# Optimization experiments

Hardware: AMD Instinct MI355X
Metric: run time of the kernel (lower is better)

The kernel has to match this reference:

```python
import jax, jax.numpy as jnp
import numpy as np

N = 30000      # num_nodes
R0 = 8         # original relations
R = 2 * R0 + 1 # with inverses + self-loop relation = 17
IN = 256
OUT = 256
E = 300000     # original triples
NB = 8         # num_bases


def setup_inputs() -> dict:
    key = jax.random.key(0)
    k1, k2, k3, k4, k5, k6 = jax.random.split(key, 6)
    s = jax.random.randint(k1, (E,), 0, N)
    r = jax.random.randint(k2, (E,), 0, R0)
    o = jax.random.randint(k3, (E,), 0, N)
    triples = jnp.stack([s, r, o], axis=1)  # [E,3] int
    features = jax.random.normal(k4, (N, IN), dtype=jnp.float32)
    bases = jax.random.normal(k5, (NB, IN, OUT), dtype=jnp.float32) * 0.02
    comps = jax.random.normal(k6, (R, NB), dtype=jnp.float32) * 0.02
    bias = jnp.zeros((OUT,), dtype=jnp.float32)
    return {"triples": triples, "features": features, "bases": bases, "comps": comps, "bias": bias}


def reference(triples, features, bases, comps, bias):
    # basis decomposition: weights[r] = sum_b comps[r,b] * bases[b]
    weights = jnp.einsum('rb,bio->rio', comps, bases)  # [R, IN, OUT]

    s, r, o = triples[:, 0], triples[:, 1], triples[:, 2]
    nodes = jnp.arange(N)
    # eval mode: self_loop_keep_prob = 1 -> all N self loops kept
    src = jnp.concatenate([s, o, nodes])                                  # [E + E + N]
    rel = jnp.concatenate([r, r + R0, jnp.full((N,), 2 * R0, r.dtype)])
    dst = jnp.concatenate([o, s, nodes])

    # horizontal stacking: adj is [N, R*N]; row = src, col = rel*N + dst
    cols = rel * N + dst
    # column normalisation (row_normalisation=False branch of sum_sparse)
    col_sums = jnp.zeros((R * N,), jnp.float32).at[cols].add(1.0)
    sums = col_sums[cols]
    # reorder: swap normalizers of original and inverse edge blocks
    sums = jnp.concatenate([sums[E:2 * E], sums[:E], sums[2 * E:]])
    vals = 1.0 / sums

    # fw[r*N + n] = features[n] @ weights[r]
    fw = jnp.einsum('ni,rio->rno', features, weights).reshape(R * N, OUT)
    msgs = vals[:, None] * fw[cols]                    # [num_edges, OUT]
    out = jnp.zeros((N, OUT), jnp.float32).at[src].add(msgs)
    return out + bias
```

## Files before the change

### kernel.cpp

```cpp
#include <hip/hip_runtime.h>


namespace {
constexpr int kN     = 30000;
constexpr int kR0    = 8;
constexpr int kNRel  = 16;
constexpr int kIN    = 256;
constexpr int kOUT   = 256;
constexpr int kE     = 300000;
constexpr int kNB    = 8;
constexpr int kKT    = kNB * kIN;
constexpr int kRows  = kN * kNRel;
constexpr int kMsgs  = 2 * kE;
constexpr int kScanBlk  = 1024;
constexpr int kNScanBlk = (kRows + kScanBlk - 1) / kScanBlk;
constexpr int kBM    = 64;
constexpr int kMB    = (kN + kBM - 1) / kBM;
constexpr int kMPad  = kMB * kBM;
constexpr int kTN    = 16;
}

typedef __bf16 bf16x8 __attribute__((ext_vector_type(8)));
typedef float  f32x4  __attribute__((ext_vector_type(4)));
typedef unsigned int u32;

static __device__ __forceinline__ ushort f2bf(float x) {
  unsigned u = __float_as_uint(x);
  u += 0x7FFF + ((u >> 16) & 1);
  return (ushort)(u >> 16);
}

static __device__ __forceinline__ void gload16(const void* g, void* l) {
  __builtin_amdgcn_global_load_lds(
      (const __attribute__((address_space(1))) u32*)g,
      (__attribute__((address_space(3))) u32*)l, 16, 0, 0);
}


__global__ void k_prep(const float* __restrict__ f, ushort* __restrict__ fb,
                       const int* __restrict__ t, int* __restrict__ deg) {
  int i = blockIdx.x * 256 + threadIdx.x;
  if (i < kN * kIN / 4) {
    float4 v = reinterpret_cast<const float4*>(f)[i];
    ushort4 p;
    p.x = f2bf(v.x); p.y = f2bf(v.y); p.z = f2bf(v.z); p.w = f2bf(v.w);
    reinterpret_cast<ushort4*>(fb)[i] = p;
  }
  if (i < kE) {
    int s = t[3*i], r = t[3*i+1], o = t[3*i+2];
    atomicAdd(&deg[s * kNRel + r], 1);
    atomicAdd(&deg[o * kNRel + kR0 + r], 1);
  }
}

__global__ void k_bt(const float* __restrict__ bases, ushort* __restrict__ Bt) {
  __shared__ float tile[16][256];
  int b = blockIdx.x;
  int t = threadIdx.x;
#pragma unroll
  for (int kk = 0; kk < 16; ++kk)
    tile[kk][t] = bases[(size_t)(b * 16 + kk) * kOUT + t];
  __syncthreads();
  char* dst = (char*)Bt + (size_t)t * 4096;
  int xr = (t & 7) << 4;
#pragma unroll
  for (int q = 0; q < 4; ++q) {
    ushort4 p;
    p.x = f2bf(tile[q*4+0][t]); p.y = f2bf(tile[q*4+1][t]);
    p.z = f2bf(tile[q*4+2][t]); p.w = f2bf(tile[q*4+3][t]);
    *reinterpret_cast<ushort4*>(dst + ((b * 32 + q * 8) ^ xr)) = p;
  }
}


__global__ void k_scan1(const int* __restrict__ deg, int* __restrict__ rp,
                        int* __restrict__ blksum) {
  __shared__ int s[256];
  int tid = threadIdx.x;
  int base = blockIdx.x * kScanBlk + tid * 4;
  int v0 = 0, v1 = 0, v2 = 0, v3 = 0;
  if (base + 3 < kRows) {
    v0 = deg[base]; v1 = deg[base+1]; v2 = deg[base+2]; v3 = deg[base+3];
  } else {
    if (base     < kRows) v0 = deg[base];
    if (base + 1 < kRows) v1 = deg[base+1];
    if (base + 2 < kRows) v2 = deg[base+2];
  }
  int t0 = v0, t1 = t0 + v1, t2 = t1 + v2, t3 = t2 + v3;
  s[tid] = t3;
  __syncthreads();
  for (int off = 1; off < 256; off <<= 1) {
    int x = 0;
    if (tid >= off) x = s[tid - off];
    __syncthreads();
    s[tid] += x;
    __syncthreads();
  }
  int excl = tid ? s[tid-1] : 0;
  if (base     < kRows) rp[base]   = excl;
  if (base + 1 < kRows) rp[base+1] = excl + t0;
  if (base + 2 < kRows) rp[base+2] = excl + t1;
  if (base + 3 < kRows) rp[base+3] = excl + t2;
  if (tid == 255) blksum[blockIdx.x] = s[255];
}

__global__ void k_scan2(int* __restrict__ blksum) {
  __shared__ int s[512];
  int tid = threadIdx.x;
  s[tid] = (tid < kNScanBlk) ? blksum[tid] : 0;
  __syncthreads();
  for (int off = 1; off < 512; off <<= 1) {
    int x = 0;
    if (tid >= off) x = s[tid - off];
    __syncthreads();
    s[tid] += x;
    __syncthreads();
  }
  if (tid < kNScanBlk) blksum[tid] = tid ? s[tid-1] : 0;
}

__global__ void k_scan3(int* __restrict__ rp, const int* __restrict__ blksum) {
  int i = blockIdx.x * 256 + threadIdx.x;
  if (i < kRows)       rp[i] += blksum[i >> 10];
  else if (i == kRows) rp[i]  = kMsgs;
}

__global__ void k_scatter(const int* __restrict__ t, const int* __restrict__ rp,
                          int* __restrict__ deg, int* __restrict__ col) {
  int m = blockIdx.x * 256 + threadIdx.x;
  if (m >= kMsgs) return;
  int e = (m < kE) ? m : m - kE;
  int s = t[3*e], r = t[3*e+1], o = t[3*e+2];
  int rr, tn, sn;
  if (m < kE) { rr = r;        tn = s; sn = o; }
  else        { rr = kR0 + r;  tn = o; sn = s; }
  int idx = tn * kNRel + rr;
  int pos = rp[idx] + (atomicSub(&deg[idx], 1) - 1);
  col[pos] = (rr << 16) | sn;
}

#define FMA4(A, S, G) \
  A.x += (S) * G.x; A.y += (S) * G.y; A.z += (S) * G.z; A.w += (S) * G.w;


__global__ __launch_bounds__(256, 4)
void k_agg1(const int* __restrict__ rp, const int* __restrict__ col,
            const float* __restrict__ feat, const ushort* __restrict__ featbf,
            const float* __restrict__ comps, ushort* __restrict__ aggb) {
  __shared__ float cvb[4][17][kNB];
  int wv   = threadIdx.x >> 6;
  int lane = threadIdx.x & 63;
  int node = blockIdx.x * 4 + wv;

  if (lane < 17) {
    float val = 0.f;
    if (lane < kNRel) {
      int idx = node * kNRel + lane;
      int d = rp[idx + 1] - rp[idx];
      val = d > 0 ? 1.0f / (float)d : 0.f;
    }
#pragma unroll
    for (int b = 0; b < kNB; ++b)
      cvb[wv][lane][b] = comps[lane * kNB + b] * val;
  }
  __syncthreads();

  int e0 = rp[node * kNRel];
  int e1 = rp[node * kNRel + kNRel];

  float4 f = *reinterpret_cast<const float4*>(feat + (size_t)node * kIN + lane * 4);
  float4 acc[kNB];
#pragma unroll
  for (int b = 0; b < kNB; ++b) {
    float cs = comps[2*kR0*kNB + b];
    acc[b].x = cs * f.x; acc[b].y = cs * f.y; acc[b].z = cs * f.z; acc[b].w = cs * f.w;
  }

  const float4* cvr = reinterpret_cast<const float4*>(&cvb[wv][0][0]);
  const int pad = (16 << 16);

  int cc0[4], cc1[4];
  uint2 g0[4];
#pragma unroll
  for (int j = 0; j < 4; ++j) {
    int ee = e0 + j;
    int v  = col[ee < kMsgs ? ee : kMsgs - 1];
    cc0[j] = ee < e1 ? v : pad;
  }
#pragma unroll
  for (int j = 0; j < 4; ++j)
    g0[j] = *reinterpret_cast<const uint2*>(featbf + (size_t)(cc0[j] & 0xFFFF) * kIN + lane * 4);
#pragma unroll
  for (int j = 0; j < 4; ++j) {
    int ee = e0 + 4 + j;
    int v  = col[ee < kMsgs ? ee : kMsgs - 1];
    cc1[j] = ee < e1 ? v : pad;
  }

#pragma unroll 2
  for (int e = e0; e < e1; e += 4) {
    uint2 g1[4];
#pragma unroll
    for (int j = 0; j < 4; ++j)
      g1[j] = *reinterpret_cast<const uint2*>(featbf + (size_t)(cc1[j] & 0xFFFF) * kIN + lane * 4);
    int cc2[4];
#pragma unroll
    for (int j = 0; j < 4; ++j) {
      int ee = e + 8 + j;
      int v  = col[ee < kMsgs ? ee : kMsgs - 1];
      cc2[j] = ee < e1 ? v : pad;
    }
#pragma unroll
    for (int j = 0; j < 4; ++j) {
      int r = cc0[j] >> 16;
      float4 c0 = cvr[r * 2];
      float4 c1 = cvr[r * 2 + 1];
      float4 gg;
      gg.x = __uint_as_float(g0[j].x << 16);
      gg.y = __uint_as_float(g0[j].x & 0xFFFF0000u);
      gg.z = __uint_as_float(g0[j].y << 16);
      gg.w = __uint_as_float(g0[j].y & 0xFFFF0000u);
      FMA4(acc[0], c0.x, gg) FMA4(acc[1], c0.y, gg)
      FMA4(acc[2], c0.z, gg) FMA4(acc[3], c0.w, gg)
      FMA4(acc[4], c1.x, gg) FMA4(acc[5], c1.y, gg)
      FMA4(acc[6], c1.z, gg) FMA4(acc[7], c1.w, gg)
    }
#pragma unroll
    for (int j = 0; j < 4; ++j) {
      cc0[j] = cc1[j]; cc1[j] = cc2[j]; g0[j] = g1[j];
    }
  }

  char* rowp = (char*)aggb + (size_t)node * 4096;
  int xr = (node & 7) << 4;
#pragma unroll
  for (int b = 0; b < kNB; ++b) {
    ushort4 p;
    p.x = f2bf(acc[b].x); p.y = f2bf(acc[b].y);
    p.z = f2bf(acc[b].z); p.w = f2bf(acc[b].w);
    *reinterpret_cast<ushort4*>(rowp + ((b * 512 + lane * 8) ^ xr)) = p;
  }
}


__global__ __launch_bounds__(512, 4)
void k_gemm(const ushort* __restrict__ aggb, const ushort* __restrict__ Bt,
            const float* __restrict__ bias, float* __restrict__ out) {
  __shared__ ushort Albs[2][kBM * 64];
  __shared__ ushort Blds[2][256 * 64];
  int tid  = threadIdx.x;
  int wv   = tid >> 6;
  int lane = tid & 63;
  int mh   = wv >> 2;
  int nq   = wv & 3;
  int l15  = lane & 15;
  int g4   = lane >> 4;
  int node0 = blockIdx.x * kBM;

  f32x4 acc[2][4];
#pragma unroll
  for (int mt = 0; mt < 2; ++mt)
#pragma unroll
    for (int nt = 0; nt < 4; ++nt) acc[mt][nt] = f32x4{0.f, 0.f, 0.f, 0.f};

  auto stage = [&](int c, int buf) {
    {
      int lin = wv * 1024 + lane * 16;
      int row = lin >> 7;
      const char* src = (const char*)aggb + (size_t)(node0 + row) * 4096
                        + c * 128 + (lin & 127);
      gload16(src, (char*)Albs[buf] + wv * 1024);
    }
#pragma unroll
    for (int i = 0; i < 4; ++i) {
      int seg = wv * 4 + i;
      int lin = seg * 1024 + lane * 16;
      int colr = lin >> 7;
      const char* src = (const char*)Bt + (size_t)colr * 4096
                        + c * 128 + (lin & 127);
      gload16(src, (char*)Blds[buf] + seg * 1024);
    }
  };

  stage(0, 0);
  asm volatile("s_waitcnt vmcnt(0)" ::: "memory");
  __syncthreads();

  int cur = 0;
  for (int c = 0; c < 32; ++c) {
    if (c + 1 < 32) stage(c + 1, cur ^ 1);
#pragma unroll
    for (int ks = 0; ks < 2; ++ks) {
      int kb = ks * 64 + g4 * 16;
      bf16x8 a[2], b[4];
#pragma unroll
      for (int mt = 0; mt < 2; ++mt) {
        int row = mh * 32 + mt * 16 + l15;
        a[mt] = *reinterpret_cast<const bf16x8*>(
            (const char*)Albs[cur] + row * 128 + (kb ^ ((row & 7) << 4)));
      }
#pragma unroll
      for (int nt = 0; nt < 4; ++nt) {
        int colr = nq * 64 + nt * 16 + l15;
        b[nt] = *reinterpret_cast<const bf16x8*>(
            (const char*)Blds[cur] + colr * 128 + (kb ^ ((colr & 7) << 4)));
      }
#pragma unroll
      for (int mt = 0; mt < 2; ++mt)
#pragma unroll
        for (int nt = 0; nt < 4; ++nt)
          acc[mt][nt] = __builtin_amdgcn_mfma_f32_16x16x32_bf16(a[mt], b[nt],
                                                                acc[mt][nt], 0, 0, 0);
    }
    asm volatile("s_waitcnt vmcnt(0)" ::: "memory");
    __syncthreads();
    cur ^= 1;
  }

#pragma unroll
  for (int nt = 0; nt < 4; ++nt) {
    int colo = nq * 64 + nt * 16 + l15;
    float bi = bias[colo];
#pragma unroll
    for (int mt = 0; mt < 2; ++mt) {
      int rbase = node0 + mh * 32 + mt * 16 + g4 * 4;
#pragma unroll
      for (int j = 0; j < 4; ++j) {
        int row = rbase + j;
        if (row < kN) out[(size_t)row * kOUT + colo] = acc[mt][nt][j] + bi;
      }
    }
  }
}


__global__ __launch_bounds__(512, 4)
void k_out_fused(const int* __restrict__ rp, const int* __restrict__ col,
                 const float* __restrict__ feat, const ushort* __restrict__ featbf,
                 const ushort* __restrict__ Bt, const float* __restrict__ comps,
                 const float* __restrict__ bias, float* __restrict__ out) {
  __shared__ ushort aggs[kTN * kKT];
  __shared__ float  cvb[kTN][17][kNB];
  int tid  = threadIdx.x;
  int wv   = tid >> 6;
  int lane = tid & 63;
  int node0 = blockIdx.x * kTN;

  for (int q = tid; q < kTN * 17; q += 512) {
    int nl = q / 17, rl = q - nl * 17;
    float val = 0.f;
    if (rl < kNRel) {
      int idx = (node0 + nl) * kNRel + rl;
      int d = rp[idx + 1] - rp[idx];
      val = d > 0 ? 1.0f / (float)d : 0.f;
    }
#pragma unroll
    for (int b = 0; b < kNB; ++b)
      cvb[nl][rl][b] = comps[rl * kNB + b] * val;
  }
  __syncthreads();

  for (int half = 0; half < 2; ++half) {
    int nl   = (wv << 1) | half;
    int node = node0 + nl;
    int e0 = rp[node * kNRel];
    int e1 = rp[node * kNRel + kNRel];

    float4 f = *reinterpret_cast<const float4*>(feat + (size_t)node * kIN + lane * 4);
    float4 acc[kNB];
#pragma unroll
    for (int b = 0; b < kNB; ++b) {
      float cs = comps[2*kR0*kNB + b];
      acc[b].x = cs * f.x; acc[b].y = cs * f.y; acc[b].z = cs * f.z; acc[b].w = cs * f.w;
    }
    const float4* cvr = reinterpret_cast<const float4*>(&cvb[nl][0][0]);
    const int pad = (16 << 16);
    int cc[4];
#pragma unroll
    for (int j = 0; j < 4; ++j) {
      int ee = e0 + j;
      int v  = col[ee < kMsgs ? ee : kMsgs - 1];
      cc[j] = ee < e1 ? v : pad;
    }
    for (int e = e0; e < e1; e += 4) {
      uint2 g[4];
#pragma unroll
      for (int j = 0; j < 4; ++j) {
        int sn = cc[j] & 0xFFFF;
        g[j] = *reinterpret_cast<const uint2*>(featbf + (size_t)sn * kIN + lane * 4);
      }
      int rr[4];
#pragma unroll
      for (int j = 0; j < 4; ++j) rr[j] = cc[j] >> 16;
#pragma unroll
      for (int j = 0; j < 4; ++j) {
        int ee = e + 4 + j;
        int v  = col[ee < kMsgs ? ee : kMsgs - 1];
        cc[j] = ee < e1 ? v : pad;
      }
#pragma unroll
      for (int j = 0; j < 4; ++j) {
        float4 c0 = cvr[rr[j] * 2];
        float4 c1 = cvr[rr[j] * 2 + 1];
        float4 gg;
        gg.x = __uint_as_float(g[j].x << 16);
        gg.y = __uint_as_float(g[j].x & 0xFFFF0000u);
        gg.z = __uint_as_float(g[j].y << 16);
        gg.w = __uint_as_float(g[j].y & 0xFFFF0000u);
        FMA4(acc[0], c0.x, gg) FMA4(acc[1], c0.y, gg)
        FMA4(acc[2], c0.z, gg) FMA4(acc[3], c0.w, gg)
        FMA4(acc[4], c1.x, gg) FMA4(acc[5], c1.y, gg)
        FMA4(acc[6], c1.z, gg) FMA4(acc[7], c1.w, gg)
      }
    }
    int xr = (nl & 7) << 4;
#pragma unroll
    for (int b = 0; b < kNB; ++b) {
      ushort4 p;
      p.x = f2bf(acc[b].x); p.y = f2bf(acc[b].y);
      p.z = f2bf(acc[b].z); p.w = f2bf(acc[b].w);
      int byteoff = nl * 4096 + ((b * 512 + lane * 8) ^ xr);
      *reinterpret_cast<ushort4*>(reinterpret_cast<char*>(aggs) + byteoff) = p;
    }
  }
  __syncthreads();

  {
    int n  = lane & 15;
    int g4 = lane >> 4;
    const char* abase = reinterpret_cast<const char*>(aggs) + n * 4096;
    int axor = (n & 7) << 4;
#pragma unroll
    for (int t = 0; t < 2; ++t) {
      int ntile = wv + t * 8;
      float bi = bias[ntile * 16 + n];
      const char* btrow = reinterpret_cast<const char*>(Bt)
                          + (size_t)(ntile * 16 + n) * 4096;
      int bxor = (n & 7) << 4;
      f32x4 acc = {0.f, 0.f, 0.f, 0.f};
#pragma unroll 4
      for (int ks = 0; ks < kKT / 32; ++ks) {
        int kb = ks * 64 + g4 * 16;
        bf16x8 af = *reinterpret_cast<const bf16x8*>(abase + (kb ^ axor));
        bf16x8 bf = *reinterpret_cast<const bf16x8*>(btrow + (kb ^ bxor));
        acc = __builtin_amdgcn_mfma_f32_16x16x32_bf16(af, bf, acc, 0, 0, 0);
      }
#pragma unroll
      for (int j = 0; j < 4; ++j) {
        int row = g4 * 4 + j;
        out[(size_t)(node0 + row) * kOUT + ntile * 16 + n] = acc[j] + bi;
      }
    }
  }
}


extern "C" void kernel_launch(void* const* d_in, const int* in_sizes, int n_in,
                              void* d_out, int out_size, void* d_ws, size_t ws_size,
                              hipStream_t stream) {
  const int*   triples = (const int*)  d_in[0];
  const float* feat    = (const float*)d_in[1];
  const float* bases   = (const float*)d_in[2];
  const float* comps   = (const float*)d_in[3];
  const float* bias    = (const float*)d_in[4];
  float* out = (float*)d_out;

  size_t featbf_b = (size_t)kN * kIN * 2;
  size_t bt_b     = (size_t)kOUT * kKT * 2;
  size_t aggb_b   = (size_t)kMPad * kKT * 2;
  size_t csr_b    = (size_t)(kRows + kRows + 1 + kMsgs + kNScanBlk) * 4;
  bool bigws = ws_size >= featbf_b + bt_b + aggb_b + csr_b + 1024;

  char* p = (char*)d_ws;
  ushort* featbf = (ushort*)p;            p += featbf_b;
  ushort* Bt     = (ushort*)p;            p += bt_b;
  ushort* aggb   = nullptr;
  if (bigws) { aggb = (ushort*)p;         p += aggb_b; }
  int* deg    = (int*)p;
  int* rp     = deg + kRows;
  int* col    = rp + kRows + 1;
  int* blksum = col + kMsgs;

  hipMemsetAsync(deg, 0, kRows * sizeof(int), stream);
  k_prep  <<<(kN * kIN / 4 + 255) / 256, 256, 0, stream>>>(feat, featbf, triples, deg);
  k_bt    <<<kKT / 16,            256, 0, stream>>>(bases, Bt);
  k_scan1 <<<kNScanBlk,           256, 0, stream>>>(deg, rp, blksum);
  k_scan2 <<<1,                   512, 0, stream>>>(blksum);
  k_scan3 <<<(kRows + 256) / 256, 256, 0, stream>>>(rp, blksum);
  k_scatter<<<(kMsgs + 255) / 256, 256, 0, stream>>>(triples, rp, deg, col);

  if (bigws) {
    k_agg1<<<kN / 4,  256, 0, stream>>>(rp, col, feat, featbf, comps, aggb);
    k_gemm<<<kMB,     512, 0, stream>>>(aggb, Bt, bias, out);
  } else {
    k_out_fused<<<kN / kTN, 512, 0, stream>>>(rp, col, feat, featbf, Bt,
                                              comps, bias, out);
  }
}
```

Measured before the change: 190.7 us.

## Use packed FP32 FMAs and shallower prefetch in aggregation kernel for higher occupancy

Rewrites the per-node aggregation loop to use inline-asm v_pk_fma_f32 on float2 accumulators, halving the FMA instruction count. It reduces the software prefetch depth from two stages to one, which lowers register pressure, and raises the launch bounds target from 4 to 6 waves. Loop bounds are made wave-uniform via readfirstlane, and the self-loop term now reads bf16 features instead of fp32. The shallower prefetch may expose more gather latency, and the bf16 self-loop input slightly changes precision.

```diff
diff --git a/kernel.cpp b/kernel.cpp
--- a/kernel.cpp
+++ b/kernel.cpp
@@ -22,6 +22,8 @@
 
 typedef __bf16 bf16x8 __attribute__((ext_vector_type(8)));
 typedef float  f32x4  __attribute__((ext_vector_type(4)));
+typedef float  f32x2  __attribute__((ext_vector_type(2)));
+typedef float  f32x4v __attribute__((ext_vector_type(4)));
 typedef unsigned int u32;
 
 static __device__ __forceinline__ ushort f2bf(float x) {
@@ -35,6 +37,11 @@
       (const __attribute__((address_space(1))) u32*)g,
       (__attribute__((address_space(3))) u32*)l, 16, 0, 0);
 }
+
+#define PKFMA_LO(ACC, G, C) \
+  asm("v_pk_fma_f32 %0, %1, %2, %0 op_sel_hi:[1,0,1]" : "+v"(ACC) : "v"(G), "v"(C))
+#define PKFMA_HI(ACC, G, C) \
+  asm("v_pk_fma_f32 %0, %1, %2, %0 op_sel:[0,1,0] op_sel_hi:[1,1,1]" : "+v"(ACC) : "v"(G), "v"(C))
 
 
 __global__ void k_prep(const float* __restrict__ f, ushort* __restrict__ fb,
@@ -143,10 +150,10 @@
   A.x += (S) * G.x; A.y += (S) * G.y; A.z += (S) * G.z; A.w += (S) * G.w;
 
 
-__global__ __launch_bounds__(256, 4)
+__global__ __launch_bounds__(256, 6)
 void k_agg1(const int* __restrict__ rp, const int* __restrict__ col,
-            const float* __restrict__ feat, const ushort* __restrict__ featbf,
-            const float* __restrict__ comps, ushort* __restrict__ aggb) {
+            const ushort* __restrict__ featbf, const float* __restrict__ comps,
+            ushort* __restrict__ aggb) {
   __shared__ float cvb[4][17][kNB];
   int wv   = threadIdx.x >> 6;
   int lane = threadIdx.x & 63;
@@ -165,69 +172,72 @@
   }
   __syncthreads();
 
-  int e0 = rp[node * kNRel];
-  int e1 = rp[node * kNRel + kNRel];
-
-  float4 f = *reinterpret_cast<const float4*>(feat + (size_t)node * kIN + lane * 4);
-  float4 acc[kNB];
-#pragma unroll
-  for (int b = 0; b < kNB; ++b) {
-    float cs = comps[2*kR0*kNB + b];
-    acc[b].x = cs * f.x; acc[b].y = cs * f.y; acc[b].z = cs * f.z; acc[b].w = cs * f.w;
-  }
-
-  const float4* cvr = reinterpret_cast<const float4*>(&cvb[wv][0][0]);
+  int se0 = __builtin_amdgcn_readfirstlane(rp[node * kNRel]);
+  int se1 = __builtin_amdgcn_readfirstlane(rp[node * kNRel + kNRel]);
+
+  f32x2 accp[2 * kNB];
+  {
+    uint2 sf = *reinterpret_cast<const uint2*>(featbf + (size_t)node * kIN + lane * 4);
+    f32x2 p01, p23;
+    p01.x = __uint_as_float(sf.x << 16);
+    p01.y = __uint_as_float(sf.x & 0xFFFF0000u);
+    p23.x = __uint_as_float(sf.y << 16);
+    p23.y = __uint_as_float(sf.y & 0xFFFF0000u);
+#pragma unroll
+    for (int b = 0; b < kNB; ++b) {
+      float cs = comps[2*kR0*kNB + b];
+      accp[2*b]     = p01 * cs;
+      accp[2*b + 1] = p23 * cs;
+    }
+  }
+
   const int pad = (16 << 16);
-
-  int cc0[4], cc1[4];
-  uint2 g0[4];
+  int voff = lane * 4;
+
+  int sc[4];
 #pragma unroll
   for (int j = 0; j < 4; ++j) {
-    int ee = e0 + j;
-    int v  = col[ee < kMsgs ? ee : kMsgs - 1];
-    cc0[j] = ee < e1 ? v : pad;
-  }
-#pragma unroll
-  for (int j = 0; j < 4; ++j)
-    g0[j] = *reinterpret_cast<const uint2*>(featbf + (size_t)(cc0[j] & 0xFFFF) * kIN + lane * 4);
-#pragma unroll
-  for (int j = 0; j < 4; ++j) {
-    int ee = e0 + 4 + j;
-    int v  = col[ee < kMsgs ? ee : kMsgs - 1];
-    cc1[j] = ee < e1 ? v : pad;
-  }
-
-#pragma unroll 2
-  for (int e = e0; e < e1; e += 4) {
-    uint2 g1[4];
-#pragma unroll
-    for (int j = 0; j < 4; ++j)
-      g1[j] = *reinterpret_cast<const uint2*>(featbf + (size_t)(cc1[j] & 0xFFFF) * kIN + lane * 4);
-    int cc2[4];
+    int ee = se0 + j;
+    int ic = ee < se1 ? ee : 0;
+    int v  = col[ic];
+    sc[j] = ee < se1 ? v : pad;
+  }
+
+  for (int e = se0; e < se1; e += 4) {
+    uint2 g[4];
 #pragma unroll
     for (int j = 0; j < 4; ++j) {
-      int ee = e + 8 + j;
-      int v  = col[ee < kMsgs ? ee : kMsgs - 1];
-      cc2[j] = ee < e1 ? v : pad;
-    }
+      const ushort* rowp = featbf + (size_t)(sc[j] & 0xFFFF) * kIN;
+      g[j] = *reinterpret_cast<const uint2*>(rowp + voff);
+    }
+    int sr[4];
+#pragma unroll
+    for (int j = 0; j < 4; ++j) sr[j] = sc[j] >> 16;
 #pragma unroll
     for (int j = 0; j < 4; ++j) {
-      int r = cc0[j] >> 16;
-      float4 c0 = cvr[r * 2];
-      float4 c1 = cvr[r * 2 + 1];
-      float4 gg;
-      gg.x = __uint_as_float(g0[j].x << 16);
-      gg.y = __uint_as_float(g0[j].x & 0xFFFF0000u);
-      gg.z = __uint_as_float(g0[j].y << 16);
-      gg.w = __uint_as_float(g0[j].y & 0xFFFF0000u);
-      FMA4(acc[0], c0.x, gg) FMA4(acc[1], c0.y, gg)
-      FMA4(acc[2], c0.z, gg) FMA4(acc[3], c0.w, gg)
-      FMA4(acc[4], c1.x, gg) FMA4(acc[5], c1.y, gg)
-      FMA4(acc[6], c1.z, gg) FMA4(acc[7], c1.w, gg)
+      int ee = e + 4 + j;
+      int ic = ee < se1 ? ee : 0;
+      int v  = col[ic];
+      sc[j] = ee < se1 ? v : pad;
     }
 #pragma unroll
     for (int j = 0; j < 4; ++j) {
-      cc0[j] = cc1[j]; cc1[j] = cc2[j]; g0[j] = g1[j];
+      f32x4v cA = *reinterpret_cast<const f32x4v*>(&cvb[wv][sr[j]][0]);
+      f32x4v cB = *reinterpret_cast<const f32x4v*>(&cvb[wv][sr[j]][4]);
+      f32x2 p01, p23;
+      p01.x = __uint_as_float(g[j].x << 16);
+      p01.y = __uint_as_float(g[j].x & 0xFFFF0000u);
+      p23.x = __uint_as_float(g[j].y << 16);
+      p23.y = __uint_as_float(g[j].y & 0xFFFF0000u);
+      f32x2 cAl = cA.lo, cAh = cA.hi, cBl = cB.lo, cBh = cB.hi;
+      PKFMA_LO(accp[0],  p01, cAl); PKFMA_LO(accp[1],  p23, cAl);
+      PKFMA_HI(accp[2],  p01, cAl); PKFMA_HI(accp[3],  p23, cAl);
+      PKFMA_LO(accp[4],  p01, cAh); PKFMA_LO(accp[5],  p23, cAh);
+      PKFMA_HI(accp[6],  p01, cAh); PKFMA_HI(accp[7],  p23, cAh);
+      PKFMA_LO(accp[8],  p01, cBl); PKFMA_LO(accp[9],  p23, cBl);
+      PKFMA_HI(accp[10], p01, cBl); PKFMA_HI(accp[11], p23, cBl);
+      PKFMA_LO(accp[12], p01, cBh); PKFMA_LO(accp[13], p23, cBh);
+      PKFMA_HI(accp[14], p01, cBh); PKFMA_HI(accp[15], p23, cBh);
     }
   }
 
@@ -236,8 +246,8 @@
 #pragma unroll
   for (int b = 0; b < kNB; ++b) {
     ushort4 p;
-    p.x = f2bf(acc[b].x); p.y = f2bf(acc[b].y);
-    p.z = f2bf(acc[b].z); p.w = f2bf(acc[b].w);
+    p.x = f2bf(accp[2*b].x);     p.y = f2bf(accp[2*b].y);
+    p.z = f2bf(accp[2*b + 1].x); p.w = f2bf(accp[2*b + 1].y);
     *reinterpret_cast<ushort4*>(rowp + ((b * 512 + lane * 8) ^ xr)) = p;
   }
 }
@@ -490,7 +500,7 @@
   k_scatter<<<(kMsgs + 255) / 256, 256, 0, stream>>>(triples, rp, deg, col);
 
   if (bigws) {
-    k_agg1<<<kN / 4,  256, 0, stream>>>(rp, col, feat, featbf, comps, aggb);
+    k_agg1<<<kN / 4,  256, 0, stream>>>(rp, col, featbf, comps, aggb);
     k_gemm<<<kMB,     512, 0, stream>>>(aggb, Bt, bias, out);
   } else {
     k_out_fused<<<kN / kTN, 512, 0, stream>>>(rp, col, feat, featbf, Bt,
```

Result: faster. 182.7 us (-4.2%).
